# Performance work log

Hardware: AMD Instinct MI355X
Metric: run time of the kernel (lower is better)

Reference implementation:

```python
import jax, jax.numpy as jnp
import numpy as np

B, S, H, L = 64, 512, 1024, 9  # batch, seq_len, hidden_size, num_labels


def setup_inputs() -> dict:
    key = jax.random.key(0)
    ks = jax.random.split(key, 8)
    hidden = jax.random.normal(ks[0], (B, S, H), dtype=jnp.float32)
    W = jax.random.normal(ks[1], (L, H), dtype=jnp.float32) * 0.02
    b = jnp.zeros((L,), dtype=jnp.float32)
    # pytorch-crf initializes transitions uniform in [-0.1, 0.1]
    start_transitions = jax.random.uniform(ks[2], (L,), jnp.float32, -0.1, 0.1)
    end_transitions = jax.random.uniform(ks[3], (L,), jnp.float32, -0.1, 0.1)
    transitions = jax.random.uniform(ks[4], (L, L), jnp.float32, -0.1, 0.1)
    labels = jax.random.randint(ks[5], (B, S), 0, L)
    # variable lengths; first timestep always valid (required by pytorch-crf)
    lengths = jax.random.randint(ks[6], (B,), S // 4, S + 1)
    mask = (jnp.arange(S)[None, :] < lengths[:, None]).astype(jnp.int32)
    return {
        "hidden": hidden, "W": W, "b": b,
        "start_transitions": start_transitions,
        "end_transitions": end_transitions,
        "transitions": transitions,
        "labels": labels, "mask": mask,
    }


def reference(hidden, W, b, start_transitions, end_transitions, transitions, labels, mask):
    # classifier: emissions [B,S,L] (fp32, matching .float() cast in the module)
    emissions = jnp.einsum("bsh,lh->bsl", hidden, W) + b
    maskf = mask.astype(emissions.dtype)

    # ---- numerator: score of the gold path ----
    emit = jnp.take_along_axis(emissions, labels[..., None], axis=-1)[..., 0]  # [B,S]
    trans_sc = transitions[labels[:, :-1], labels[:, 1:]]                       # [B,S-1]
    score = (start_transitions[labels[:, 0]]
             + jnp.sum(emit * maskf, axis=1)
             + jnp.sum(trans_sc * maskf[:, 1:], axis=1))
    seq_ends = jnp.sum(mask, axis=1) - 1                     # last valid index per example
    last_tags = labels[jnp.arange(labels.shape[0]), seq_ends]
    score = score + end_transitions[last_tags]

    # ---- denominator: log partition via masked forward recurrence ----
    alpha0 = start_transitions[None, :] + emissions[:, 0]    # [B,L]
    em_t = jnp.swapaxes(emissions, 0, 1)[1:]                 # [S-1,B,L]
    mk_t = jnp.swapaxes(mask, 0, 1)[1:].astype(bool)         # [S-1,B]

    def step(alpha, xs):
        e_t, m_t = xs
        # broadcast: alpha[b,i] + transitions[i,j] + e_t[b,j]
        nxt = jax.scipy.special.logsumexp(
            alpha[:, :, None] + transitions[None, :, :] + e_t[:, None, :], axis=1)
        alpha = jnp.where(m_t[:, None], nxt, alpha)
        return alpha, None

    alpha, _ = jax.lax.scan(step, alpha0, (em_t, mk_t))
    logZ = jax.scipy.special.logsumexp(alpha + end_transitions[None, :], axis=1)  # [B]

    llh = score - logZ
    loss = -jnp.mean(llh)  # reduction='mean', negated in the module
    return loss
```

## Files before the change

### kernel.cpp

```cpp
#include <hip/hip_runtime.h>
#include <hip/hip_bf16.h>

#define LOG2E 1.4426950408889634f
#define LN2   0.6931471805599453f

constexpr int Bn = 64, Sn = 512, Hn = 1024, Ln = 9;
constexpr int CL = 24;
constexpr int NC = 22;

typedef __attribute__((ext_vector_type(8))) short short8v;
typedef __attribute__((ext_vector_type(4))) float f32x4;

__device__ __forceinline__ float fexp2(float x) {
    float r; asm("v_exp_f32 %0, %1" : "=v"(r) : "v"(x)); return r;
}
__device__ __forceinline__ float flog2(float x) {
    float r; asm("v_log_f32 %0, %1" : "=v"(r) : "v"(x)); return r;
}
__device__ __forceinline__ unsigned cvtpk(float lo, float hi) {
    unsigned r; asm("v_cvt_pk_bf16_f32 %0, %1, %2" : "=v"(r) : "v"(lo), "v"(hi)); return r;
}
__device__ __forceinline__ float max9(const float* s) {
    return fmaxf(fmaxf(fmaxf(s[0], s[1]), fmaxf(s[2], s[3])),
                 fmaxf(fmaxf(s[4], s[5]), fmaxf(s[6], fmaxf(s[7], s[8]))));
}

__global__ __launch_bounds__(256) void emis_kernel(
    const float* __restrict__ hidden, const float* __restrict__ W,
    const float* __restrict__ bias, float* __restrict__ emis,
    float* __restrict__ out0)
{
    __shared__ __align__(16) unsigned short wfrag[32][64][8];
    const int tid = threadIdx.x, lane = tid & 63, w = tid >> 6;

    if (blockIdx.x == 0 && tid == 0) out0[0] = 0.f;

    for (int f = tid; f < 32 * 64; f += 256) {
        const int s = f >> 6, l = f & 63;
        const int j = l & 15, k0 = s * 32 + ((l >> 4) << 3);
        uint4 pk = {0u, 0u, 0u, 0u};
        if (j < Ln) {
            float4 a = *(const float4*)(W + j * Hn + k0);
            float4 b = *(const float4*)(W + j * Hn + k0 + 4);
            pk.x = cvtpk(a.x, a.y); pk.y = cvtpk(a.z, a.w);
            pk.z = cvtpk(b.x, b.y); pk.w = cvtpk(b.z, b.w);
        }
        *(uint4*)&wfrag[s][l][0] = pk;
    }
    __syncthreads();

    const int row0 = blockIdx.x * 64 + w * 16;
    const float* hptr = hidden + (size_t)(row0 + (lane & 15)) * Hn + ((lane >> 4) << 3);

    f32x4 acc = {0.f, 0.f, 0.f, 0.f};
    #pragma unroll 4
    for (int s = 0; s < 32; ++s) {
        float4 a0 = *(const float4*)(hptr + s * 32);
        float4 a1 = *(const float4*)(hptr + s * 32 + 4);
        uint4 ap;
        ap.x = cvtpk(a0.x, a0.y); ap.y = cvtpk(a0.z, a0.w);
        ap.z = cvtpk(a1.x, a1.y); ap.w = cvtpk(a1.z, a1.w);
        short8v A  = *(short8v*)&ap;
        short8v Bv = *(const short8v*)&wfrag[s][lane][0];
        acc = __builtin_amdgcn_mfma_f32_16x16x32_bf16(A, Bv, acc, 0, 0, 0);
    }

    const int col = lane & 15;
    if (col < Ln) {
        const float bv = bias[col];
        #pragma unroll
        for (int r = 0; r < 4; ++r) {
            const int row = ((lane >> 4) << 2) + r;
            emis[(size_t)(row0 + row) * Ln + col] = acc[r] + bv;
        }
    }
}

__global__ __launch_bounds__(256, 1) void crf_kernel(
    const float* __restrict__ emis, const float* __restrict__ st,
    const float* __restrict__ et,   const float* __restrict__ T,
    const int* __restrict__ labels, const int* __restrict__ mask,
    float* __restrict__ out)
{
    __shared__ __align__(16) float e_lds[Sn * Ln];
    __shared__ float M_lds[NC][Ln][10];
    __shared__ float part[4];
    __shared__ int   sl_sh;

    const int b    = blockIdx.x;
    const int tid  = threadIdx.x;
    const int w    = tid >> 6;
    const int lane = tid & 63;

    {
        const float4* src = (const float4*)(emis + (size_t)b * Sn * Ln);
        float4* dst = (float4*)e_lds;
        for (int i = tid; i < (Sn * Ln) / 4; i += 256) dst[i] = src[i];
    }
    float E[Ln][Ln];
    #pragma unroll
    for (int k = 0; k < Ln; ++k)
        #pragma unroll
        for (int j = 0; j < Ln; ++j)
            E[k][j] = fexp2(T[k * Ln + j] * LOG2E);
    if (w == 3) {
        const int* mb = mask + b * Sn;
        int s = 0;
        #pragma unroll
        for (int r = 0; r < Sn / 64; ++r) s += mb[lane + r * 64];
        #pragma unroll
        for (int off = 32; off; off >>= 1) s += __shfl_xor(s, off);
        if (lane == 0) sl_sh = s;
    }
    __syncthreads();

    const int sl    = sl_sh;
    const int nreal = (sl - 1 + CL - 1) / CL;

    {
        const int ul = lane / 9;
        const int i  = lane - ul * 9;
        const int c  = w * 7 + ul;
        const int t0 = 1 + c * CL;
        if (ul < 7 && c < nreal) {
            const int nst = min(CL, sl - t0);
            float u[Ln];
            {
                const float* e0 = e_lds + t0 * Ln;
                #pragma unroll
                for (int j = 0; j < Ln; ++j)
                    u[j] = E[i][j] * fexp2(fmaf(e0[j], LOG2E, -4.f));
            }
            float extra = 0.f;
            for (int s = 1; s < nst; ++s) {
                const float* es = e_lds + (t0 + s) * Ln;
                float e2[Ln];
                #pragma unroll
                for (int j = 0; j < Ln; ++j) e2[j] = es[j];
                float v[Ln];
                #pragma unroll
                for (int j = 0; j < Ln; ++j) v[j] = 0.f;
                #pragma unroll
                for (int kk = 0; kk < Ln; ++kk) {
                    const float uk = u[kk];
                    #pragma unroll
                    for (int j = 0; j < Ln; ++j)
                        v[j] = fmaf(uk, E[kk][j], v[j]);
                }
                #pragma unroll
                for (int j = 0; j < Ln; ++j)
                    u[j] = v[j] * fexp2(fmaf(e2[j], LOG2E, -4.f));
                if (s == 12) {
                    float m  = max9(u);
                    float iv = 1.f / m;
                    #pragma unroll
                    for (int j = 0; j < Ln; ++j) u[j] *= iv;
                    extra = flog2(m);
                }
            }
            #pragma unroll
            for (int j = 0; j < Ln; ++j)
                M_lds[c][i][j] = flog2(u[j]) + extra + 4.f * (float)nst;
        }
    }
    __syncthreads();

    float logZ = 0.f;
    if (w == 0) {
        const int j9 = lane < Ln ? lane : Ln - 1;
        float al[Ln];
        #pragma unroll
        for (int j = 0; j < Ln; ++j) al[j] = (st[j] + e_lds[j]) * LOG2E;
        for (int c = 0; c < nreal; ++c) {
            float s[Ln];
            #pragma unroll
            for (int k = 0; k < Ln; ++k) s[k] = al[k] + M_lds[c][k][j9];
            float p = max9(s);
            float sum = fexp2(s[0] - p);
            #pragma unroll
            for (int k = 1; k < Ln; ++k) sum += fexp2(s[k] - p);
            float aj = p + flog2(sum);
            #pragma unroll
            for (int k = 0; k < Ln; ++k) al[k] = __shfl(aj, k);
        }
        float z[Ln];
        #pragma unroll
        for (int j = 0; j < Ln; ++j) z[j] = al[j] + et[j] * LOG2E;
        float p = max9(z);
        float sum = fexp2(z[0] - p);
        #pragma unroll
        for (int j = 1; j < Ln; ++j) sum += fexp2(z[j] - p);
        logZ = (p + flog2(sum)) * LN2;
    } else {
        const int* lb = labels + b * Sn;
        float sc = 0.f;
        for (int t = (w - 1) * 64 + lane; t < sl; t += 192) {
            int lt = lb[t];
            sc += e_lds[t * Ln + lt];
            if (t >= 1) sc += T[lb[t - 1] * Ln + lt];
        }
        #pragma unroll
        for (int off = 32; off; off >>= 1) sc += __shfl_xor(sc, off);
        if (w == 1 && lane == 0) sc += st[lb[0]] + et[lb[sl - 1]];
        if (lane == 0) part[w - 1] = sc;
    }
    __syncthreads();

    if (w == 0 && lane == 0) {
        float llh = part[0] + part[1] + part[2] - logZ;
        atomicAdd(out, llh * (-1.f / 64.f));
    }
}

extern "C" void kernel_launch(void* const* d_in, const int* in_sizes, int n_in,
                              void* d_out, int out_size, void* d_ws, size_t ws_size,
                              hipStream_t stream) {
    const float* hidden = (const float*)d_in[0];
    const float* W      = (const float*)d_in[1];
    const float* bias   = (const float*)d_in[2];
    const float* st     = (const float*)d_in[3];
    const float* et     = (const float*)d_in[4];
    const float* T      = (const float*)d_in[5];
    const int*   labels = (const int*)d_in[6];
    const int*   mask   = (const int*)d_in[7];

    float* emis = (float*)d_ws;
    float* outp = (float*)d_out;

    emis_kernel<<<512, 256, 0, stream>>>(hidden, W, bias, emis, outp);
    crf_kernel<<<Bn, 256, 0, stream>>>(emis, st, et, T, labels, mask, outp);
}
```

Measured before the change: 43.76 us.

## Prefetch hidden rows with nontemporal loads and move length reduction into GEMM kernel

The emission GEMM now issues nontemporal loads of the hidden tile before the barrier and keeps a 4-deep register prefetch ring, so global latency overlaps with the W fragment staging and the MFMA loop. The mask-length reduction moves into the first kernel and is written to workspace, which removes a wave's serial job from the CRF kernel. In the CRF kernel, chunk length changes to 25 with 21 chunks, and the gold-path score is computed by the fourth wave in parallel with the chunk matrix products, which drops one barrier. The cost is higher register pressure from the prefetch ring and an extra workspace buffer.

```diff
diff --git a/kernel.cpp b/kernel.cpp
--- a/kernel.cpp
+++ b/kernel.cpp
@@ -5,8 +5,8 @@
 #define LN2   0.6931471805599453f
 
 constexpr int Bn = 64, Sn = 512, Hn = 1024, Ln = 9;
-constexpr int CL = 24;
-constexpr int NC = 22;
+constexpr int CL = 25;
+constexpr int NC = 21;
 
 typedef __attribute__((ext_vector_type(8))) short short8v;
 typedef __attribute__((ext_vector_type(4))) float f32x4;
@@ -24,16 +24,20 @@
     return fmaxf(fmaxf(fmaxf(s[0], s[1]), fmaxf(s[2], s[3])),
                  fmaxf(fmaxf(s[4], s[5]), fmaxf(s[6], fmaxf(s[7], s[8]))));
 }
+__device__ __forceinline__ f32x4 nt4(const float* p) {
+    return __builtin_nontemporal_load((const f32x4*)p);
+}
 
 __global__ __launch_bounds__(256) void emis_kernel(
     const float* __restrict__ hidden, const float* __restrict__ W,
-    const float* __restrict__ bias, float* __restrict__ emis,
-    float* __restrict__ out0)
+    const float* __restrict__ bias,   const int* __restrict__ mask,
+    float* __restrict__ emis, int* __restrict__ slbuf, float* __restrict__ out0)
 {
     __shared__ __align__(16) unsigned short wfrag[32][64][8];
     const int tid = threadIdx.x, lane = tid & 63, w = tid >> 6;
-
-    if (blockIdx.x == 0 && tid == 0) out0[0] = 0.f;
+    const int bid = blockIdx.x, b = bid >> 3, rb = bid & 7;
+
+    if (bid == 0 && tid == 0) out0[0] = 0.f;
 
     for (int f = tid; f < 32 * 64; f += 256) {
         const int s = f >> 6, l = f & 63;
@@ -41,28 +45,47 @@
         uint4 pk = {0u, 0u, 0u, 0u};
         if (j < Ln) {
             float4 a = *(const float4*)(W + j * Hn + k0);
-            float4 b = *(const float4*)(W + j * Hn + k0 + 4);
+            float4 c = *(const float4*)(W + j * Hn + k0 + 4);
             pk.x = cvtpk(a.x, a.y); pk.y = cvtpk(a.z, a.w);
-            pk.z = cvtpk(b.x, b.y); pk.w = cvtpk(b.z, b.w);
+            pk.z = cvtpk(c.x, c.y); pk.w = cvtpk(c.z, c.w);
         }
         *(uint4*)&wfrag[s][l][0] = pk;
     }
+
+    const int row0 = bid * 64 + w * 16;
+    const float* hptr = hidden + (size_t)(row0 + (lane & 15)) * Hn + ((lane >> 4) << 3);
+    f32x4 A[4][2];
+    #pragma unroll
+    for (int s = 0; s < 4; ++s) {
+        A[s][0] = nt4(hptr + s * 32);
+        A[s][1] = nt4(hptr + s * 32 + 4);
+    }
+
+    if (rb == 0 && w == 0) {
+        const int* mb = mask + b * Sn;
+        int s = 0;
+        #pragma unroll
+        for (int r = 0; r < Sn / 64; ++r) s += mb[lane + r * 64];
+        #pragma unroll
+        for (int off = 32; off; off >>= 1) s += __shfl_xor(s, off);
+        if (lane == 0) slbuf[b] = s;
+    }
     __syncthreads();
-
-    const int row0 = blockIdx.x * 64 + w * 16;
-    const float* hptr = hidden + (size_t)(row0 + (lane & 15)) * Hn + ((lane >> 4) << 3);
 
     f32x4 acc = {0.f, 0.f, 0.f, 0.f};
     #pragma unroll 4
     for (int s = 0; s < 32; ++s) {
-        float4 a0 = *(const float4*)(hptr + s * 32);
-        float4 a1 = *(const float4*)(hptr + s * 32 + 4);
+        f32x4 a0 = A[s & 3][0], a1 = A[s & 3][1];
+        if (s < 28) {
+            A[s & 3][0] = nt4(hptr + (s + 4) * 32);
+            A[s & 3][1] = nt4(hptr + (s + 4) * 32 + 4);
+        }
         uint4 ap;
-        ap.x = cvtpk(a0.x, a0.y); ap.y = cvtpk(a0.z, a0.w);
-        ap.z = cvtpk(a1.x, a1.y); ap.w = cvtpk(a1.z, a1.w);
-        short8v A  = *(short8v*)&ap;
+        ap.x = cvtpk(a0[0], a0[1]); ap.y = cvtpk(a0[2], a0[3]);
+        ap.z = cvtpk(a1[0], a1[1]); ap.w = cvtpk(a1[2], a1[3]);
+        short8v Av = *(short8v*)&ap;
         short8v Bv = *(const short8v*)&wfrag[s][lane][0];
-        acc = __builtin_amdgcn_mfma_f32_16x16x32_bf16(A, Bv, acc, 0, 0, 0);
+        acc = __builtin_amdgcn_mfma_f32_16x16x32_bf16(Av, Bv, acc, 0, 0, 0);
     }
 
     const int col = lane & 15;
@@ -79,13 +102,12 @@
 __global__ __launch_bounds__(256, 1) void crf_kernel(
     const float* __restrict__ emis, const float* __restrict__ st,
     const float* __restrict__ et,   const float* __restrict__ T,
-    const int* __restrict__ labels, const int* __restrict__ mask,
+    const int* __restrict__ labels, const int* __restrict__ slbuf,
     float* __restrict__ out)
 {
     __shared__ __align__(16) float e_lds[Sn * Ln];
     __shared__ float M_lds[NC][Ln][10];
-    __shared__ float part[4];
-    __shared__ int   sl_sh;
+    __shared__ float part[1];
 
     const int b    = blockIdx.x;
     const int tid  = threadIdx.x;
@@ -97,32 +119,24 @@
         float4* dst = (float4*)e_lds;
         for (int i = tid; i < (Sn * Ln) / 4; i += 256) dst[i] = src[i];
     }
+    const int sl = slbuf[b];
     float E[Ln][Ln];
     #pragma unroll
     for (int k = 0; k < Ln; ++k)
         #pragma unroll
         for (int j = 0; j < Ln; ++j)
             E[k][j] = fexp2(T[k * Ln + j] * LOG2E);
-    if (w == 3) {
-        const int* mb = mask + b * Sn;
-        int s = 0;
-        #pragma unroll
-        for (int r = 0; r < Sn / 64; ++r) s += mb[lane + r * 64];
-        #pragma unroll
-        for (int off = 32; off; off >>= 1) s += __shfl_xor(s, off);
-        if (lane == 0) sl_sh = s;
-    }
     __syncthreads();
 
-    const int sl    = sl_sh;
     const int nreal = (sl - 1 + CL - 1) / CL;
 
-    {
+    float logZ = 0.f;
+    if (w < 3) {
         const int ul = lane / 9;
         const int i  = lane - ul * 9;
         const int c  = w * 7 + ul;
         const int t0 = 1 + c * CL;
-        if (ul < 7 && c < nreal) {
+        if (ul < 7 && t0 < sl) {
             const int nst = min(CL, sl - t0);
             float u[Ln];
             {
@@ -162,10 +176,20 @@
             for (int j = 0; j < Ln; ++j)
                 M_lds[c][i][j] = flog2(u[j]) + extra + 4.f * (float)nst;
         }
+    } else {
+        const int* lb = labels + b * Sn;
+        float sc = 0.f;
+        for (int t = lane; t < sl; t += 64) {
+            int lt = lb[t];
+            sc += e_lds[t * Ln + lt];
+            if (t >= 1) sc += T[lb[t - 1] * Ln + lt];
+        }
+        #pragma unroll
+        for (int off = 32; off; off >>= 1) sc += __shfl_xor(sc, off);
+        if (lane == 0) part[0] = sc + st[lb[0]] + et[lb[sl - 1]];
     }
     __syncthreads();
 
-    float logZ = 0.f;
     if (w == 0) {
         const int j9 = lane < Ln ? lane : Ln - 1;
         float al[Ln];
@@ -191,24 +215,11 @@
         #pragma unroll
         for (int j = 1; j < Ln; ++j) sum += fexp2(z[j] - p);
         logZ = (p + flog2(sum)) * LN2;
-    } else {
-        const int* lb = labels + b * Sn;
-        float sc = 0.f;
-        for (int t = (w - 1) * 64 + lane; t < sl; t += 192) {
-            int lt = lb[t];
-            sc += e_lds[t * Ln + lt];
-            if (t >= 1) sc += T[lb[t - 1] * Ln + lt];
-        }
-        #pragma unroll
-        for (int off = 32; off; off >>= 1) sc += __shfl_xor(sc, off);
-        if (w == 1 && lane == 0) sc += st[lb[0]] + et[lb[sl - 1]];
-        if (lane == 0) part[w - 1] = sc;
-    }
-    __syncthreads();
-
-    if (w == 0 && lane == 0) {
-        float llh = part[0] + part[1] + part[2] - logZ;
-        atomicAdd(out, llh * (-1.f / 64.f));
+
+        if (lane == 0) {
+            float llh = part[0] - logZ;
+            atomicAdd(out, llh * (-1.f / 64.f));
+        }
     }
 }
 
@@ -224,9 +235,10 @@
     const int*   labels = (const int*)d_in[6];
     const int*   mask   = (const int*)d_in[7];
 
-    float* emis = (float*)d_ws;
-    float* outp = (float*)d_out;
-
-    emis_kernel<<<512, 256, 0, stream>>>(hidden, W, bias, emis, outp);
-    crf_kernel<<<Bn, 256, 0, stream>>>(emis, st, et, T, labels, mask, outp);
-}
+    float* emis  = (float*)d_ws;
+    int*   slbuf = (int*)(emis + (size_t)Bn * Sn * Ln);
+    float* outp  = (float*)d_out;
+
+    emis_kernel<<<512, 256, 0, stream>>>(hidden, W, bias, mask, emis, slbuf, outp);
+    crf_kernel<<<Bn, 256, 0, stream>>>(emis, st, et, T, labels, slbuf, outp);
+}
```

Result: slower. 49.48 us (+13.1%).
